# Performance work log

Measured on AMD Instinct MI355X. Metric: run time of the kernel, lower is better.

The kernel has to match this reference:

```python
import jax, jax.numpy as jnp
import numpy as np
from jax import lax

SEQ, B, F, L = 32, 32, 64, 256
OC = 128          # out_channels
K = 5
PAD = (K - 1) // 2
GROUPS = 4 * OC // 32  # GroupNorm groups = 16
EPS = 1e-5


def group_norm(x, w, b):
    # x: (B, C, L); normalize over each group's (C//G, L) slice
    bsz, c, l = x.shape
    xg = x.reshape(bsz, GROUPS, -1)
    mu = jnp.mean(xg, axis=-1, keepdims=True)
    var = jnp.var(xg, axis=-1, keepdims=True)
    xg = (xg - mu) * lax.rsqrt(var + EPS)
    return xg.reshape(bsz, c, l) * w[None, :, None] + b[None, :, None]


def setup_inputs() -> dict:
    key = jax.random.key(0)
    k1, k2, k3 = jax.random.split(key, 3)
    fan_in = (F + OC) * K
    return {
        "inputs": jax.random.normal(k1, (SEQ, B, F, L), dtype=jnp.float32),
        "conv_w": jax.random.normal(k2, (4 * OC, F + OC, K), dtype=jnp.float32) / np.sqrt(fan_in),
        "conv_b": jax.random.normal(k3, (4 * OC,), dtype=jnp.float32) * 0.01,
        "gn_w": jnp.ones((4 * OC,), dtype=jnp.float32),
        "gn_b": jnp.zeros((4 * OC,), dtype=jnp.float32),
    }


def reference(inputs, conv_w, conv_b, gn_w, gn_b):
    bsz, sub_len = inputs.shape[1], inputs.shape[3]
    hx0 = jnp.zeros((bsz, OC, sub_len), dtype=inputs.dtype)
    cx0 = jnp.zeros((bsz, OC, sub_len), dtype=inputs.dtype)

    def step(carry, x):
        hx, cx = carry
        combined = jnp.concatenate([x, hx], axis=1)  # (B, F+OC, L)
        gates = lax.conv_general_dilated(
            combined, conv_w, window_strides=(1,), padding=[(PAD, PAD)],
            dimension_numbers=("NCH", "OIH", "NCH"))
        gates = gates + conv_b[None, :, None]
        gates = group_norm(gates, gn_w, gn_b)
        i, f, g, o = jnp.split(gates, 4, axis=1)
        cy = jax.nn.sigmoid(f) * cx + jax.nn.sigmoid(i) * jnp.tanh(g)
        hy = jax.nn.sigmoid(o) * jnp.tanh(cy)
        return (hy, cy), hy

    (hy, cy), outputs = lax.scan(step, (hx0, cx0), inputs)
    return outputs, (hy, cy)
```

## Files before the change

kernel.cpp:

```cpp
#include <hip/hip_runtime.h>

typedef unsigned short u16;
typedef unsigned int u32;
typedef unsigned long long u64;
typedef __attribute__((ext_vector_type(4))) float f32x4;
typedef __attribute__((ext_vector_type(8))) short s16x8;
typedef __attribute__((ext_vector_type(4))) int i32x4;

#define EPS 1e-5f

__device__ __forceinline__ u16 f2bf(float f) {
  unsigned u = __float_as_uint(f);
  return (u16)((u + 0x7fffu + ((u >> 16) & 1u)) >> 16);
}
__device__ __forceinline__ float sigm(float x) { return 1.0f / (1.0f + __expf(-x)); }
__device__ __forceinline__ float tanh_f(float x) {
  float e = __expf(-2.0f * fabsf(x));
  float r = (1.0f - e) / (1.0f + e);
  return copysignf(r, x);
}
__device__ __forceinline__ void gl_lds16(const void* g, void* l) {
  __builtin_amdgcn_global_load_lds(
      (const __attribute__((address_space(1))) u32*)g,
      (__attribute__((address_space(3))) u32*)l, 16, 0, 0);
}

__global__ __launch_bounds__(256) void k_setup(
    const float* __restrict__ cw, u16* __restrict__ Wpk,
    const float* __restrict__ x, u16* __restrict__ xT,
    i32x4* __restrict__ hTz, i32x4* __restrict__ cxz, i32x4* __restrict__ flz) {
  const int bid = blockIdx.x, tid = threadIdx.x;
  __shared__ __align__(16) u16 ltile[256 * 72];
  if (bid < 1920) {
    int idx = bid * 256 + tid;
    int f = idx >> 9, r = idx & 511;
    int lane = r >> 3, j = r & 7;
    int of = f & 31, tk = f >> 5;
    int kk = tk % 6, tap = tk / 6;
    int o = (of << 4) + (lane & 15);
    int c = (kk << 5) + ((lane >> 4) << 3) + j;
    Wpk[idx] = f2bf(cw[(o * 192 + c) * 5 + tap]);
  } else if (bid < 2944) {
    int tb = bid - 1920;
    const float* src = x + tb * (64 * 256);
    for (int it = 0; it < 64; ++it) {
      int idx = it * 256 + tid;
      int c = idx >> 8, l = idx & 255;
      ltile[l * 72 + c] = f2bf(src[idx]);
    }
    __syncthreads();
    char* dst = (char*)(xT + tb * 16896);
    i32x4 z = {0, 0, 0, 0};
    for (int i = tid; i < 2112; i += 256) {
      int r = i >> 3, ch = i & 7;
      i32x4 v = z;
      if (r >= 2 && r < 258) v = *(const i32x4*)(ltile + (r - 2) * 72 + ch * 8);
      *(i32x4*)(dst + r * 128 + ((ch * 16) ^ ((r & 7) << 4))) = v;
    }
  } else {
    int base = (bid - 2944) * 256 + tid;
    i32x4 z = {0, 0, 0, 0};
    for (int i = base; i < 270336; i += 131072) hTz[i] = z;
    for (int i = base; i < 262144; i += 131072) cxz[i] = z;
    for (int i = base; i < 2048;   i += 131072) flz[i] = z;
  }
}

__global__ __launch_bounds__(512) void k_step(
    const u16* __restrict__ Wpk, const u16* __restrict__ xT, u16* __restrict__ hT,
    const float* __restrict__ cb, const float* __restrict__ gnw, const float* __restrict__ gnb,
    float* __restrict__ cx, float* __restrict__ out,
    float* __restrict__ stats, int* __restrict__ flags, int t) {
  const int bid = blockIdx.x;
  const int b = bid & 31, lh = (bid >> 5) & 1, cs = bid >> 6;
  const int L0 = lh << 7;
  const int tid = threadIdx.x, wave = tid >> 6, lane = tid & 63;
  const int wm = wave & 1, wl = wave >> 1;
  const int l15 = lane & 15, q = lane >> 4;
  const int cgrp = q << 4;

  __shared__ __align__(16) char ldsx[16896];
  __shared__ __align__(16) char ldsh[33792];
  __shared__ __align__(16) char hl[8192];
  __shared__ float red[8][4][2];
  __shared__ float blkstat[8];
  __shared__ float smu[4], srs[4];

  const u16* hTr = hT + (t & 1) * 1081344;
  u16* hTw = hT + ((t + 1) & 1) * 1081344;

  {
    const char* gx = (const char*)(xT + ((t << 5) + b) * 16896) + (lh << 14);
    for (int i = tid; i < 1056; i += 512) gl_lds16(gx + (i << 4), ldsx + (i << 4));
    const char* gh = (const char*)hTr + b * 67584 + (lh << 15);
    for (int i = tid; i < 2112; i += 512) gl_lds16(gh + (i << 4), ldsh + (i << 4));
  }
  asm volatile("s_waitcnt vmcnt(0)" ::: "memory");
  __syncthreads();

  f32x4 zero4 = {0.f, 0.f, 0.f, 0.f};
  f32x4 acc[4][2];
  #pragma unroll
  for (int g = 0; g < 4; ++g) { acc[g][0] = zero4; acc[g][1] = zero4; }

  const s16x8* Wv = (const s16x8*)Wpk;
  for (int tap = 0; tap < 5; ++tap) {
    #pragma unroll
    for (int kk = 0; kk < 6; ++kk) {
      const int cc = tap * 6 + kk;
      s16x8 av[4], bv[2];
      #pragma unroll
      for (int g = 0; g < 4; ++g) {
        const int of = (g << 3) + (cs << 1) + wm;
        av[g] = Wv[(((cc << 5) + of) << 6) + lane];
      }
      #pragma unroll
      for (int ni = 0; ni < 2; ++ni) {
        const int rr = (wl << 5) + (ni << 4) + l15 + tap;
        const int sw = (rr & 7) << 4;
        bv[ni] = (kk < 2)
          ? *(const s16x8*)(ldsx + (rr << 7) + (((kk << 6) + cgrp) ^ sw))
          : *(const s16x8*)(ldsh + (rr << 8) + ((((kk - 2) << 6) + cgrp) ^ sw));
      }
      #pragma unroll
      for (int g = 0; g < 4; ++g) {
        acc[g][0] = __builtin_amdgcn_mfma_f32_16x16x32_bf16(av[g], bv[0], acc[g][0], 0, 0, 0);
        acc[g][1] = __builtin_amdgcn_mfma_f32_16x16x32_bf16(av[g], bv[1], acc[g][1], 0, 0, 0);
      }
    }
  }

  const int chq = (cs << 5) + (wm << 4) + (q << 2);
  float sum4[4], sq4[4];
  #pragma unroll
  for (int g = 0; g < 4; ++g) {
    const f32x4 bias = *(const f32x4*)(cb + (g << 7) + chq);
    sum4[g] = 0.f; sq4[g] = 0.f;
    #pragma unroll
    for (int ni = 0; ni < 2; ++ni)
      #pragma unroll
      for (int r = 0; r < 4; ++r) {
        float v = acc[g][ni][r] + bias[r];
        acc[g][ni][r] = v;
        sum4[g] += v; sq4[g] += v * v;
      }
  }
  f32x4 w4[4], b4[4];
  float cxv[2][4];
  #pragma unroll
  for (int g = 0; g < 4; ++g) {
    w4[g] = *(const f32x4*)(gnw + (g << 7) + chq);
    b4[g] = *(const f32x4*)(gnb + (g << 7) + chq);
  }
  #pragma unroll
  for (int ni = 0; ni < 2; ++ni) {
    const int l = L0 + (wl << 5) + (ni << 4) + l15;
    #pragma unroll
    for (int r = 0; r < 4; ++r)
      cxv[ni][r] = cx[(b << 15) + ((chq + r) << 8) + l];
  }
  #pragma unroll
  for (int off = 1; off < 64; off <<= 1) {
    #pragma unroll
    for (int g = 0; g < 4; ++g) {
      sum4[g] += __shfl_xor(sum4[g], off);
      sq4[g]  += __shfl_xor(sq4[g], off);
    }
  }
  if (lane == 0) {
    #pragma unroll
    for (int g = 0; g < 4; ++g) { red[wave][g][0] = sum4[g]; red[wave][g][1] = sq4[g]; }
  }
  __syncthreads();
  if (tid < 8) {
    const int g = tid >> 1, j = tid & 1;
    float v = 0.f;
    #pragma unroll
    for (int w = 0; w < 8; ++w) v += red[w][g][j];
    blkstat[tid] = v;
  }
  __syncthreads();

  const int sidx = (((t << 5) + b) << 3) + (cs << 1) + lh;
  if (tid == 0) {
    float* sp = stats + (sidx << 3);
    #pragma unroll
    for (int j = 0; j < 8; ++j)
      __hip_atomic_store(sp + j, blkstat[j], __ATOMIC_RELAXED, __HIP_MEMORY_SCOPE_AGENT);
    __hip_atomic_store(&flags[sidx], 1, __ATOMIC_RELEASE, __HIP_MEMORY_SCOPE_AGENT);
    while (__hip_atomic_load(&flags[sidx ^ 1], __ATOMIC_RELAXED, __HIP_MEMORY_SCOPE_AGENT) == 0)
      __builtin_amdgcn_s_sleep(2);
    __builtin_amdgcn_fence(__ATOMIC_ACQUIRE, "agent");
    const float* pe = stats + ((sidx & ~1) << 3);
    const float* po = stats + ((sidx | 1) << 3);
    const float inv = 1.0f / 8192.0f;
    #pragma unroll
    for (int g = 0; g < 4; ++g) {
      float s = __hip_atomic_load(pe + (g << 1), __ATOMIC_RELAXED, __HIP_MEMORY_SCOPE_AGENT)
              + __hip_atomic_load(po + (g << 1), __ATOMIC_RELAXED, __HIP_MEMORY_SCOPE_AGENT);
      float qv = __hip_atomic_load(pe + (g << 1) + 1, __ATOMIC_RELAXED, __HIP_MEMORY_SCOPE_AGENT)
               + __hip_atomic_load(po + (g << 1) + 1, __ATOMIC_RELAXED, __HIP_MEMORY_SCOPE_AGENT);
      float m = s * inv;
      smu[g] = m;
      srs[g] = rsqrtf(qv * inv - m * m + EPS);
    }
  }
  __syncthreads();

  const float mu0 = smu[0], mu1 = smu[1], mu2 = smu[2], mu3 = smu[3];
  const float rs0 = srs[0], rs1 = srs[1], rs2 = srs[2], rs3 = srs[3];
  float* outp = out + (((t << 5) + b) << 15);
  #pragma unroll
  for (int ni = 0; ni < 2; ++ni) {
    const int l = L0 + (wl << 5) + (ni << 4) + l15;
    const int ll = l - L0;
    u16 hp[4];
    #pragma unroll
    for (int r = 0; r < 4; ++r) {
      const int c = chq + r;
      float vi = (acc[0][ni][r] - mu0) * rs0 * w4[0][r] + b4[0][r];
      float vf = (acc[1][ni][r] - mu1) * rs1 * w4[1][r] + b4[1][r];
      float vg = (acc[2][ni][r] - mu2) * rs2 * w4[2][r] + b4[2][r];
      float vo = (acc[3][ni][r] - mu3) * rs3 * w4[3][r] + b4[3][r];
      float cyv = sigm(vf) * cxv[ni][r] + sigm(vi) * tanh_f(vg);
      float hyv = sigm(vo) * tanh_f(cyv);
      const int ci = (c << 8) + l;
      cx[(b << 15) + ci] = cyv;
      outp[ci] = hyv;
      hp[r] = f2bf(hyv);
      if (t == 31) {
        out[33554432 + (b << 15) + ci] = hyv;
        out[34603008 + (b << 15) + ci] = cyv;
      }
    }
    *(u64*)(hl + (ll << 6) + (((wm << 5) + (q << 3)) ^ ((ll & 3) << 4))) =
        *(const u64*)hp;
  }
  __syncthreads();

  {
    const int ll = tid >> 2, k = tid & 3;
    const int row = L0 + ll + 2;
    i32x4 v = *(const i32x4*)(hl + (ll << 6) + ((k << 4) ^ ((ll & 3) << 4)));
    char* dst = (char*)hTw + b * 67584 + (row << 8) +
                ((((cs << 2) + k) << 4) ^ ((row & 7) << 4));
    *(i32x4*)dst = v;
  }
}

extern "C" void kernel_launch(void* const* d_in, const int* in_sizes, int n_in,
                              void* d_out, int out_size, void* d_ws, size_t ws_size,
                              hipStream_t stream) {
  const float* x  = (const float*)d_in[0];
  const float* cw = (const float*)d_in[1];
  const float* cb = (const float*)d_in[2];
  const float* gw = (const float*)d_in[3];
  const float* gb = (const float*)d_in[4];
  float* out = (float*)d_out;
  char* ws = (char*)d_ws;

  u16*   Wpk   = (u16*)(ws);
  u16*   xT    = (u16*)(ws + 983040);
  u16*   hT    = (u16*)(ws + 35586048);
  float* cx    = (float*)(ws + 39911424);
  float* stats = (float*)(ws + 44105728);
  int*   flags = (int*)(ws + 44367872);

  k_setup<<<3456, 256, 0, stream>>>(cw, Wpk, x, xT, (i32x4*)hT, (i32x4*)cx, (i32x4*)flags);
  for (int t = 0; t < 32; ++t)
    k_step<<<256, 512, 0, stream>>>(Wpk, xT, hT, cb, gw, gb, cx, out, stats, flags, t);
}
```

Baseline: 675.0 us.

## Give each block the full sequence length to drop cross-block GroupNorm sync

Each step block now covers all 256 positions instead of half, so GroupNorm statistics are reduced inside the block. The inter-block flag spin-wait and the global stats exchange are removed. The grid halves to 128 blocks, and each wave accumulates a 4x4 MFMA tile. In exchange, only half the CUs are used per step, and the larger LDS footprint (~118KB) and register count limit each CU to one block.

Result: slower. 707.6 us (+4.8%).

```diff
diff --git a/kernel.cpp b/kernel.cpp
--- a/kernel.cpp
+++ b/kernel.cpp
@@ -28,7 +28,7 @@
 __global__ __launch_bounds__(256) void k_setup(
     const float* __restrict__ cw, u16* __restrict__ Wpk,
     const float* __restrict__ x, u16* __restrict__ xT,
-    i32x4* __restrict__ hTz, i32x4* __restrict__ cxz, i32x4* __restrict__ flz) {
+    i32x4* __restrict__ hTz, i32x4* __restrict__ cxz) {
   const int bid = blockIdx.x, tid = threadIdx.x;
   __shared__ __align__(16) u16 ltile[256 * 72];
   if (bid < 1920) {
@@ -62,71 +62,69 @@
     i32x4 z = {0, 0, 0, 0};
     for (int i = base; i < 270336; i += 131072) hTz[i] = z;
     for (int i = base; i < 262144; i += 131072) cxz[i] = z;
-    for (int i = base; i < 2048;   i += 131072) flz[i] = z;
-  }
-}
-
-__global__ __launch_bounds__(512) void k_step(
+  }
+}
+
+__global__ __launch_bounds__(512, 1) void k_step(
     const u16* __restrict__ Wpk, const u16* __restrict__ xT, u16* __restrict__ hT,
     const float* __restrict__ cb, const float* __restrict__ gnw, const float* __restrict__ gnb,
-    float* __restrict__ cx, float* __restrict__ out,
-    float* __restrict__ stats, int* __restrict__ flags, int t) {
+    float* __restrict__ cx, float* __restrict__ out, int t) {
   const int bid = blockIdx.x;
-  const int b = bid & 31, lh = (bid >> 5) & 1, cs = bid >> 6;
-  const int L0 = lh << 7;
+  const int b = bid & 31, cs = bid >> 5;
   const int tid = threadIdx.x, wave = tid >> 6, lane = tid & 63;
   const int wm = wave & 1, wl = wave >> 1;
   const int l15 = lane & 15, q = lane >> 4;
   const int cgrp = q << 4;
 
-  __shared__ __align__(16) char ldsx[16896];
-  __shared__ __align__(16) char ldsh[33792];
-  __shared__ __align__(16) char hl[8192];
+  __shared__ __align__(16) char ldsx[33792];
+  __shared__ __align__(16) char ldsh[67584];
+  __shared__ __align__(16) char hl[16384];
   __shared__ float red[8][4][2];
-  __shared__ float blkstat[8];
   __shared__ float smu[4], srs[4];
 
   const u16* hTr = hT + (t & 1) * 1081344;
   u16* hTw = hT + ((t + 1) & 1) * 1081344;
 
   {
-    const char* gx = (const char*)(xT + ((t << 5) + b) * 16896) + (lh << 14);
-    for (int i = tid; i < 1056; i += 512) gl_lds16(gx + (i << 4), ldsx + (i << 4));
-    const char* gh = (const char*)hTr + b * 67584 + (lh << 15);
-    for (int i = tid; i < 2112; i += 512) gl_lds16(gh + (i << 4), ldsh + (i << 4));
+    const char* gx = (const char*)(xT + ((t << 5) + b) * 16896);
+    for (int i = tid; i < 2112; i += 512) gl_lds16(gx + (i << 4), ldsx + (i << 4));
+    const char* gh = (const char*)hTr + b * 67584;
+    for (int i = tid; i < 4224; i += 512) gl_lds16(gh + (i << 4), ldsh + (i << 4));
   }
   asm volatile("s_waitcnt vmcnt(0)" ::: "memory");
   __syncthreads();
 
   f32x4 zero4 = {0.f, 0.f, 0.f, 0.f};
-  f32x4 acc[4][2];
-  #pragma unroll
-  for (int g = 0; g < 4; ++g) { acc[g][0] = zero4; acc[g][1] = zero4; }
+  f32x4 acc[4][4];
+  #pragma unroll
+  for (int g = 0; g < 4; ++g)
+    #pragma unroll
+    for (int ni = 0; ni < 4; ++ni) acc[g][ni] = zero4;
 
   const s16x8* Wv = (const s16x8*)Wpk;
   for (int tap = 0; tap < 5; ++tap) {
     #pragma unroll
     for (int kk = 0; kk < 6; ++kk) {
       const int cc = tap * 6 + kk;
-      s16x8 av[4], bv[2];
+      s16x8 av[4], bv[4];
       #pragma unroll
       for (int g = 0; g < 4; ++g) {
         const int of = (g << 3) + (cs << 1) + wm;
         av[g] = Wv[(((cc << 5) + of) << 6) + lane];
       }
       #pragma unroll
-      for (int ni = 0; ni < 2; ++ni) {
-        const int rr = (wl << 5) + (ni << 4) + l15 + tap;
+      for (int ni = 0; ni < 4; ++ni) {
+        const int rr = (wl << 6) + (ni << 4) + l15 + tap;
         const int sw = (rr & 7) << 4;
         bv[ni] = (kk < 2)
           ? *(const s16x8*)(ldsx + (rr << 7) + (((kk << 6) + cgrp) ^ sw))
           : *(const s16x8*)(ldsh + (rr << 8) + ((((kk - 2) << 6) + cgrp) ^ sw));
       }
       #pragma unroll
-      for (int g = 0; g < 4; ++g) {
-        acc[g][0] = __builtin_amdgcn_mfma_f32_16x16x32_bf16(av[g], bv[0], acc[g][0], 0, 0, 0);
-        acc[g][1] = __builtin_amdgcn_mfma_f32_16x16x32_bf16(av[g], bv[1], acc[g][1], 0, 0, 0);
-      }
+      for (int g = 0; g < 4; ++g)
+        #pragma unroll
+        for (int ni = 0; ni < 4; ++ni)
+          acc[g][ni] = __builtin_amdgcn_mfma_f32_16x16x32_bf16(av[g], bv[ni], acc[g][ni], 0, 0, 0);
     }
   }
 
@@ -137,7 +135,7 @@
     const f32x4 bias = *(const f32x4*)(cb + (g << 7) + chq);
     sum4[g] = 0.f; sq4[g] = 0.f;
     #pragma unroll
-    for (int ni = 0; ni < 2; ++ni)
+    for (int ni = 0; ni < 4; ++ni)
       #pragma unroll
       for (int r = 0; r < 4; ++r) {
         float v = acc[g][ni][r] + bias[r];
@@ -146,15 +144,15 @@
       }
   }
   f32x4 w4[4], b4[4];
-  float cxv[2][4];
+  float cxv[4][4];
   #pragma unroll
   for (int g = 0; g < 4; ++g) {
     w4[g] = *(const f32x4*)(gnw + (g << 7) + chq);
     b4[g] = *(const f32x4*)(gnb + (g << 7) + chq);
   }
   #pragma unroll
-  for (int ni = 0; ni < 2; ++ni) {
-    const int l = L0 + (wl << 5) + (ni << 4) + l15;
+  for (int ni = 0; ni < 4; ++ni) {
+    const int l = (wl << 6) + (ni << 4) + l15;
     #pragma unroll
     for (int r = 0; r < 4; ++r)
       cxv[ni][r] = cx[(b << 15) + ((chq + r) << 8) + l];
@@ -172,38 +170,14 @@
     for (int g = 0; g < 4; ++g) { red[wave][g][0] = sum4[g]; red[wave][g][1] = sq4[g]; }
   }
   __syncthreads();
-  if (tid < 8) {
-    const int g = tid >> 1, j = tid & 1;
-    float v = 0.f;
-    #pragma unroll
-    for (int w = 0; w < 8; ++w) v += red[w][g][j];
-    blkstat[tid] = v;
-  }
-  __syncthreads();
-
-  const int sidx = (((t << 5) + b) << 3) + (cs << 1) + lh;
-  if (tid == 0) {
-    float* sp = stats + (sidx << 3);
-    #pragma unroll
-    for (int j = 0; j < 8; ++j)
-      __hip_atomic_store(sp + j, blkstat[j], __ATOMIC_RELAXED, __HIP_MEMORY_SCOPE_AGENT);
-    __hip_atomic_store(&flags[sidx], 1, __ATOMIC_RELEASE, __HIP_MEMORY_SCOPE_AGENT);
-    while (__hip_atomic_load(&flags[sidx ^ 1], __ATOMIC_RELAXED, __HIP_MEMORY_SCOPE_AGENT) == 0)
-      __builtin_amdgcn_s_sleep(2);
-    __builtin_amdgcn_fence(__ATOMIC_ACQUIRE, "agent");
-    const float* pe = stats + ((sidx & ~1) << 3);
-    const float* po = stats + ((sidx | 1) << 3);
+  if (tid < 4) {
+    float s = 0.f, qv = 0.f;
+    #pragma unroll
+    for (int w = 0; w < 8; ++w) { s += red[w][tid][0]; qv += red[w][tid][1]; }
     const float inv = 1.0f / 8192.0f;
-    #pragma unroll
-    for (int g = 0; g < 4; ++g) {
-      float s = __hip_atomic_load(pe + (g << 1), __ATOMIC_RELAXED, __HIP_MEMORY_SCOPE_AGENT)
-              + __hip_atomic_load(po + (g << 1), __ATOMIC_RELAXED, __HIP_MEMORY_SCOPE_AGENT);
-      float qv = __hip_atomic_load(pe + (g << 1) + 1, __ATOMIC_RELAXED, __HIP_MEMORY_SCOPE_AGENT)
-               + __hip_atomic_load(po + (g << 1) + 1, __ATOMIC_RELAXED, __HIP_MEMORY_SCOPE_AGENT);
-      float m = s * inv;
-      smu[g] = m;
-      srs[g] = rsqrtf(qv * inv - m * m + EPS);
-    }
+    float m = s * inv;
+    smu[tid] = m;
+    srs[tid] = rsqrtf(qv * inv - m * m + EPS);
   }
   __syncthreads();
 
@@ -211,9 +185,8 @@
   const float rs0 = srs[0], rs1 = srs[1], rs2 = srs[2], rs3 = srs[3];
   float* outp = out + (((t << 5) + b) << 15);
   #pragma unroll
-  for (int ni = 0; ni < 2; ++ni) {
-    const int l = L0 + (wl << 5) + (ni << 4) + l15;
-    const int ll = l - L0;
+  for (int ni = 0; ni < 4; ++ni) {
+    const int l = (wl << 6) + (ni << 4) + l15;
     u16 hp[4];
     #pragma unroll
     for (int r = 0; r < 4; ++r) {
@@ -233,14 +206,15 @@
         out[34603008 + (b << 15) + ci] = cyv;
       }
     }
-    *(u64*)(hl + (ll << 6) + (((wm << 5) + (q << 3)) ^ ((ll & 3) << 4))) =
+    *(u64*)(hl + (l << 6) + (((wm << 5) + (q << 3)) ^ ((l & 3) << 4))) =
         *(const u64*)hp;
   }
   __syncthreads();
 
-  {
-    const int ll = tid >> 2, k = tid & 3;
-    const int row = L0 + ll + 2;
+  #pragma unroll
+  for (int i = tid; i < 1024; i += 512) {
+    const int ll = i >> 2, k = i & 3;
+    const int row = ll + 2;
     i32x4 v = *(const i32x4*)(hl + (ll << 6) + ((k << 4) ^ ((ll & 3) << 4)));
     char* dst = (char*)hTw + b * 67584 + (row << 8) +
                 ((((cs << 2) + k) << 4) ^ ((row & 7) << 4));
@@ -259,14 +233,12 @@
   float* out = (float*)d_out;
   char* ws = (char*)d_ws;
 
-  u16*   Wpk   = (u16*)(ws);
-  u16*   xT    = (u16*)(ws + 983040);
-  u16*   hT    = (u16*)(ws + 35586048);
-  float* cx    = (float*)(ws + 39911424);
-  float* stats = (float*)(ws + 44105728);
-  int*   flags = (int*)(ws + 44367872);
-
-  k_setup<<<3456, 256, 0, stream>>>(cw, Wpk, x, xT, (i32x4*)hT, (i32x4*)cx, (i32x4*)flags);
+  u16*   Wpk = (u16*)(ws);
+  u16*   xT  = (u16*)(ws + 983040);
+  u16*   hT  = (u16*)(ws + 35586048);
+  float* cx  = (float*)(ws + 39911424);
+
+  k_setup<<<3456, 256, 0, stream>>>(cw, Wpk, x, xT, (i32x4*)hT, (i32x4*)cx);
   for (int t = 0; t < 32; ++t)
-    k_step<<<256, 512, 0, stream>>>(Wpk, xT, hT, cb, gw, gb, cx, out, stats, flags, t);
-}
+    k_step<<<128, 512, 0, stream>>>(Wpk, xT, hT, cb, gw, gb, cx, out, t);
+}
```
